# Performance work log

Measured on AMD Instinct MI355X. Metric: run time of the kernel, lower is better.

Reference implementation:

```python
import jax, jax.numpy as jnp
import numpy as np

B, C, H, W = 4, 256, 64, 64
CP = C // 4  # embedding_channels, k=4 hardcoded
# branch index -> (key-stream i, query/value-stream j); streams: 0=t,1=b,2=m
IIDX = np.array([0, 0, 0, 1, 1, 1, 2, 2, 2])  # which stream feeds k
JIDX = np.array([0, 1, 2, 0, 1, 2, 0, 1, 2])  # which stream feeds q and v


def setup_inputs() -> dict:
    key = jax.random.key(0)
    ks = jax.random.split(key, 6)
    scale = 0.05
    return {
        "t": jax.random.normal(ks[0], (B, C, H, W), jnp.float32),
        "b": jax.random.normal(ks[1], (B, C, H, W), jnp.float32),
        "m": jax.random.normal(ks[2], (B, C, H, W), jnp.float32),
        "W_qkv": jax.random.normal(ks[3], (9, C, C), jnp.float32) * scale,
        "W_red": jax.random.normal(ks[4], (9, CP, C), jnp.float32) * scale,
        "W_rec": jax.random.normal(ks[5], (9, C, CP), jnp.float32) * scale,
    }


def _pool(x):
    # ChannelAttention: global avg pool + global max pool -> [B, C']
    return jnp.mean(x, axis=(2, 3)) + jnp.max(x, axis=(2, 3))


def _channel_attention(q, k, v, w_red, w_rec):
    # q,k,v: [B,C,H,W]; w_red: [C',C]; w_rec: [C,C']
    ori = q + k + v
    red = lambda x: jax.nn.relu(jnp.einsum("bchw,ec->behw", x, w_red))
    qr, kr, vr = red(q), red(k), red(v)
    f = _pool(kr)  # key   -> [B,C']
    g = _pool(qr)  # query -> [B,C']
    h = _pool(vr)  # value -> [B,C']
    # s = f^T g : [B,C',C']; softmax over dim=1 (rows), per torch nn.Softmax(dim=1)
    s = f[:, :, None] * g[:, None, :]
    beta = jax.nn.softmax(s, axis=1)
    vout = jnp.einsum("bi,bij->bj", h, beta)  # [B,C']
    # recovery 1x1 conv on [B,C',1,1]; bilinear upsample from 1x1 == broadcast
    o = jax.nn.sigmoid(jnp.einsum("be,ce->bc", vout, w_rec))  # [B,C]
    return o[:, :, None, None] * ori


def reference(t, b, m, W_qkv, W_red, W_rec):
    x = jnp.stack([t, b, m])  # [3,B,C,H,W]
    Wp = W_qkv.reshape(3, 3, C, C)  # [stream, (q,k,v), C_out, C_in]
    proj = jnp.einsum("sbchw,sjec->sjbehw", x, Wp)  # [3,3,B,C,H,W]
    Q, K, V = proj[:, 0], proj[:, 1], proj[:, 2]  # each [3,B,C,H,W]
    q9, k9, v9 = Q[JIDX], K[IIDX], V[JIDX]  # [9,B,C,H,W]
    outs = jax.vmap(_channel_attention)(q9, k9, v9, W_red, W_rec)
    return outs.sum(axis=0)
```

## Files before the change

### kernel.cpp

```cpp
#include <hip/hip_runtime.h>

#define Bn 4
#define Cn 256
#define HWn 4096
#define CPn 64
#define MP 640

typedef unsigned short u16;
typedef unsigned int u32;

using short8  = __attribute__((ext_vector_type(8))) short;
using floatx4 = __attribute__((ext_vector_type(4))) float;

static __device__ __forceinline__ u16 f2bf(float f) {
    union { float f; u32 u; } v; v.f = f;
    u32 r = (v.u + 0x7FFFu + ((v.u >> 16) & 1u)) >> 16;
    return (u16)r;
}

static __device__ __forceinline__ void gld16(const u16* g, u16* l) {
    __builtin_amdgcn_global_load_lds(
        (const __attribute__((address_space(1))) u32*)g,
        (__attribute__((address_space(3))) u32*)l, 16, 0, 0);
}


__global__ __launch_bounds__(256) void convert_transpose(
    const float* __restrict__ Tt, const float* __restrict__ Bt, const float* __restrict__ Mt,
    u16* __restrict__ xT)
{
    const int s  = blockIdx.z, b = blockIdx.y;
    const int ct = blockIdx.x & 3, hwt = blockIdx.x >> 2;
    const int c0 = ct * 64, hw0 = hwt * 64;
    const float* X = (s == 0 ? Tt : (s == 1 ? Bt : Mt)) + (size_t)b * Cn * HWn;

    __shared__ u16 T[64][72];
    const int t = threadIdx.x;
    const int cl = t >> 2, q = t & 3;

    const float* src = X + (size_t)(c0 + cl) * HWn + hw0 + q * 16;
    #pragma unroll
    for (int u = 0; u < 4; ++u) {
        const float4 v = *(const float4*)(src + u * 4);
        T[cl][q * 16 + u * 4 + 0] = f2bf(v.x);
        T[cl][q * 16 + u * 4 + 1] = f2bf(v.y);
        T[cl][q * 16 + u * 4 + 2] = f2bf(v.z);
        T[cl][q * 16 + u * 4 + 3] = f2bf(v.w);
    }
    __syncthreads();

    const int wl = t >> 2;
    u16* dst = xT + ((size_t)((s * Bn + b) * HWn) + hw0 + wl) * Cn + c0 + q * 16;
    #pragma unroll
    for (int u = 0; u < 2; ++u) {
        u32 w0 = (u32)T[q * 16 + u * 8 + 0][wl] | ((u32)T[q * 16 + u * 8 + 1][wl] << 16);
        u32 w1 = (u32)T[q * 16 + u * 8 + 2][wl] | ((u32)T[q * 16 + u * 8 + 3][wl] << 16);
        u32 w2 = (u32)T[q * 16 + u * 8 + 4][wl] | ((u32)T[q * 16 + u * 8 + 5][wl] << 16);
        u32 w3 = (u32)T[q * 16 + u * 8 + 6][wl] | ((u32)T[q * 16 + u * 8 + 7][wl] << 16);
        uint4 pk = {w0, w1, w2, w3};
        *(uint4*)(dst + u * 8) = pk;
    }
}

__global__ __launch_bounds__(256) void compose_red(
    const float* __restrict__ Wqkv, const float* __restrict__ Wred,
    u16* __restrict__ CWp)
{
    const int s  = blockIdx.z;
    const int tt = blockIdx.y / 3, m3 = blockIdx.y % 3;
    const int c0 = blockIdx.x * 64;
    const int idx = (tt == 1) ? (3 * s + m3) : (3 * m3 + s);

    const float* A = Wred + (size_t)idx * CPn * Cn;
    const float* Bm = Wqkv + (size_t)(3 * s + tt) * Cn * Cn;

    __shared__ float As[16][64];
    __shared__ float Bs[16][64];
    const int t = threadIdx.x;
    const int ty = t >> 4, tx = t & 15;
    float acc[4][4] = {};

    for (int k0 = 0; k0 < Cn; k0 += 16) {
        {
            const int r = t >> 2, eq = (t & 3) * 4;
            const float4 a = *(const float4*)(A + (size_t)r * Cn + k0 + eq);
            As[eq + 0][r] = a.x; As[eq + 1][r] = a.y; As[eq + 2][r] = a.z; As[eq + 3][r] = a.w;
        }
        {
            const int r = t >> 4, cq = (t & 15) * 4;
            *(float4*)(&Bs[r][cq]) = *(const float4*)(Bm + (size_t)(k0 + r) * Cn + c0 + cq);
        }
        __syncthreads();
        #pragma unroll
        for (int k = 0; k < 16; ++k) {
            const float4 a4 = *(const float4*)(&As[k][ty * 4]);
            const float4 b4 = *(const float4*)(&Bs[k][tx * 4]);
            const float a[4] = {a4.x, a4.y, a4.z, a4.w};
            const float bb[4] = {b4.x, b4.y, b4.z, b4.w};
            #pragma unroll
            for (int i = 0; i < 4; ++i)
                #pragma unroll
                for (int j = 0; j < 4; ++j)
                    acc[i][j] = fmaf(a[i], bb[j], acc[i][j]);
        }
        __syncthreads();
    }

    u16* out = CWp + (size_t)s * MP * Cn;
    #pragma unroll
    for (int i = 0; i < 4; ++i) {
        const int row = tt * 192 + m3 * 64 + ty * 4 + i;
        unsigned long long pk =
            (unsigned long long)f2bf(acc[i][0]) |
            ((unsigned long long)f2bf(acc[i][1]) << 16) |
            ((unsigned long long)f2bf(acc[i][2]) << 32) |
            ((unsigned long long)f2bf(acc[i][3]) << 48);
        *(unsigned long long*)(out + (size_t)row * Cn + c0 + tx * 4) = pk;
    }
}

__global__ __launch_bounds__(256, 2) void redpool_mfma(
    const u16* __restrict__ xT, const u16* __restrict__ CWp,
    float* __restrict__ Psum, float* __restrict__ Pmax)
{
    const int s  = blockIdx.z;
    const int mt = blockIdx.x >> 7, nt = blockIdx.x & 127;
    const int m0 = mt * 128, n0 = nt * 128;

    const u16* Ap = CWp + (size_t)s * MP * Cn;
    const u16* Bp = xT + (size_t)s * Bn * HWn * Cn;

    __shared__ __align__(16) u16 As[32 * 512];
    __shared__ __align__(16) u16 Bs[32 * 512];

    const int t = threadIdx.x;
    const int w = t >> 6, lane = t & 63;
    const int l15 = lane & 15, q = lane >> 4;
    const int rb = (w >> 1) * 64, cb = (w & 1) * 64;

    floatx4 acc[4][4] = {};

    #pragma unroll
    for (int it = 0; it < 2; ++it) {
        const int k0 = it * 128;
        const u16* Asrc = Ap + (size_t)(m0 + l15) * Cn + k0 + q * 8;
        const u16* Bsrc = Bp + (size_t)(n0 + l15) * Cn + k0 + q * 8;
        #pragma unroll
        for (int pi = 0; pi < 8; ++pi) {
            const int p = w * 8 + pi;
            const size_t roff = (size_t)((p >> 2) * 16);
            gld16(Asrc + roff * Cn + (p & 3) * 32, &As[p * 512]);
            gld16(Bsrc + roff * Cn + (p & 3) * 32, &Bs[p * 512]);
        }
        __syncthreads();
        #pragma unroll
        for (int kk = 0; kk < 4; ++kk) {
            short8 af[4], bf[4];
            #pragma unroll
            for (int i = 0; i < 4; ++i)
                af[i] = *(const short8*)&As[((((w >> 1) * 4 + i) << 2) + kk) * 512 + lane * 8];
            #pragma unroll
            for (int j = 0; j < 4; ++j)
                bf[j] = *(const short8*)&Bs[((((w & 1) * 4 + j) << 2) + kk) * 512 + lane * 8];
            #pragma unroll
            for (int i = 0; i < 4; ++i)
                #pragma unroll
                for (int j = 0; j < 4; ++j)
                    acc[i][j] = __builtin_amdgcn_mfma_f32_16x16x32_bf16(af[i], bf[j], acc[i][j], 0, 0, 0);
        }
        __syncthreads();
    }

    float* Lsum = (float*)As;
    float* Lmax = Lsum + 256;
    const int wi = w & 1;
    #pragma unroll
    for (int i = 0; i < 4; ++i) {
        #pragma unroll
        for (int r = 0; r < 4; ++r) {
            float rs = 0.f, rm = 0.f;
            #pragma unroll
            for (int j = 0; j < 4; ++j) {
                const float v = fmaxf(acc[i][j][r], 0.f);
                rs += v; rm = fmaxf(rm, v);
            }
            #pragma unroll
            for (int off = 1; off < 16; off <<= 1) {
                rs += __shfl_xor(rs, off);
                rm = fmaxf(rm, __shfl_xor(rm, off));
            }
            if (l15 == 0) {
                const int lr = rb + 16 * i + q * 4 + r;
                Lsum[wi * 128 + lr] = rs;
                Lmax[wi * 128 + lr] = rm;
            }
        }
    }
    __syncthreads();
    if (t < 128) {
        const int R = m0 + t;
        const int b = nt >> 5, chunk = nt & 31;
        const size_t o = (((size_t)s * MP + R) * Bn + b) * 32 + chunk;
        Psum[o] = Lsum[t] + Lsum[128 + t];
        Pmax[o] = fmaxf(Lmax[t], Lmax[128 + t]);
    }
}

__global__ __launch_bounds__(256) void attn_small(
    const float* __restrict__ Psum, const float* __restrict__ Pmax,
    const float* __restrict__ Wrec,
    float* __restrict__ coefA, float* __restrict__ coefK)
{
    const int idx = blockIdx.x / Bn;
    const int bb  = blockIdx.x % Bn;
    __shared__ float ff[CPn], gg[CPn], hh[CPn], vout[CPn];
    const int t = threadIdx.x;

    if (t < CPn) {
        float v[3];
        #pragma unroll
        for (int tt = 0; tt < 3; ++tt) {
            const int s_ = (tt == 1) ? idx / 3 : idx % 3;
            const int m3 = (tt == 1) ? idx % 3 : idx / 3;
            const int R  = tt * 192 + m3 * 64 + t;
            const size_t base = (((size_t)s_ * MP + R) * Bn + bb) * 32;
            float sm = 0.f, mx = 0.f;
            #pragma unroll
            for (int u = 0; u < 32; ++u) {
                sm += Psum[base + u];
                mx = fmaxf(mx, Pmax[base + u]);
            }
            v[tt] = sm * (1.0f / HWn) + mx;
        }
        gg[t] = v[0];
        ff[t] = v[1];
        hh[t] = v[2];
    }
    __syncthreads();

    if (t < CPn) {
        const float gj = gg[t];
        float mx = -1e30f;
        for (int i = 0; i < CPn; ++i) mx = fmaxf(mx, ff[i] * gj);
        float den = 0.f, num = 0.f;
        for (int i = 0; i < CPn; ++i) {
            const float e = expf(ff[i] * gj - mx);
            den += e;
            num += hh[i] * e;
        }
        vout[t] = num / den;
    }
    __syncthreads();

    {
        const float* wr = Wrec + ((size_t)idx * Cn + t) * CPn;
        float a = 0.f;
        for (int e = 0; e < CPn; ++e) a += vout[e] * wr[e];
        const float o = 1.0f / (1.0f + expf(-a));
        const int sj = idx % 3;
        const int si = idx / 3;
        atomicAdd(coefA + (sj * Bn + bb) * Cn + t, o);
        atomicAdd(coefK + (si * Bn + bb) * Cn + t, o);
    }
}

__global__ __launch_bounds__(256) void build_M(
    const float* __restrict__ Wqkv,
    const float* __restrict__ coefA, const float* __restrict__ coefK,
    u16* __restrict__ Mm)
{
    const int s = blockIdx.x >> 8, m = blockIdx.x & 255;
    const int b = blockIdx.y;
    const int t = threadIdx.x;
    const float cA = coefA[(s * Bn + b) * Cn + m];
    const float cK = coefK[(s * Bn + b) * Cn + m];
    const float wq = Wqkv[((size_t)(3 * s + 0) * Cn + m) * Cn + t];
    const float wk = Wqkv[((size_t)(3 * s + 1) * Cn + m) * Cn + t];
    const float wv = Wqkv[((size_t)(3 * s + 2) * Cn + m) * Cn + t];
    Mm[((size_t)(b * 256 + m)) * 768 + s * 256 + t] = f2bf(cA * (wq + wv) + cK * wk);
}

__global__ __launch_bounds__(256, 2) void final_mfma(
    const u16* __restrict__ xT, const u16* __restrict__ Mm,
    float* __restrict__ out)
{
    const int b  = blockIdx.y;
    const int mt = blockIdx.x >> 5, nt = blockIdx.x & 31;
    const int m0 = mt * 128, n0 = nt * 128;

    __shared__ __align__(16) u16 As[32 * 512];
    __shared__ __align__(16) u16 Bs[32 * 512];

    const int t = threadIdx.x;
    const int w = t >> 6, lane = t & 63;
    const int l15 = lane & 15, q = lane >> 4;
    const int rb = (w >> 1) * 64, cb = (w & 1) * 64;

    const u16* Apb = Mm + (size_t)(b * 256 + m0) * 768;

    floatx4 acc[4][4] = {};

    for (int k0 = 0; k0 < 768; k0 += 128) {
        const int s = k0 >> 8, c0 = k0 & 255;
        const u16* Asrc = Apb + (size_t)l15 * 768 + k0 + q * 8;
        const u16* Bsrc = xT + ((size_t)((s * Bn + b) * HWn) + n0 + l15) * Cn + c0 + q * 8;
        #pragma unroll
        for (int pi = 0; pi < 8; ++pi) {
            const int p = w * 8 + pi;
            const size_t roff = (size_t)((p >> 2) * 16);
            gld16(Asrc + roff * 768 + (p & 3) * 32, &As[p * 512]);
            gld16(Bsrc + roff * Cn + (p & 3) * 32, &Bs[p * 512]);
        }
        __syncthreads();
        #pragma unroll
        for (int kk = 0; kk < 4; ++kk) {
            short8 af[4], bf[4];
            #pragma unroll
            for (int i = 0; i < 4; ++i)
                af[i] = *(const short8*)&As[((((w >> 1) * 4 + i) << 2) + kk) * 512 + lane * 8];
            #pragma unroll
            for (int j = 0; j < 4; ++j)
                bf[j] = *(const short8*)&Bs[((((w & 1) * 4 + j) << 2) + kk) * 512 + lane * 8];
            #pragma unroll
            for (int i = 0; i < 4; ++i)
                #pragma unroll
                for (int j = 0; j < 4; ++j)
                    acc[i][j] = __builtin_amdgcn_mfma_f32_16x16x32_bf16(af[i], bf[j], acc[i][j], 0, 0, 0);
        }
        __syncthreads();
    }

    #pragma unroll
    for (int i = 0; i < 4; ++i)
        #pragma unroll
        for (int j = 0; j < 4; ++j)
            #pragma unroll
            for (int r = 0; r < 4; ++r) {
                const int row = m0 + rb + i * 16 + q * 4 + r;
                const int col = n0 + cb + j * 16 + l15;
                out[((size_t)(b * 256) + row) * HWn + col] = acc[i][j][r];
            }
}

extern "C" void kernel_launch(void* const* d_in, const int* in_sizes, int n_in,
                              void* d_out, int out_size, void* d_ws, size_t ws_size,
                              hipStream_t stream)
{
    const float* Tt   = (const float*)d_in[0];
    const float* Bt   = (const float*)d_in[1];
    const float* Mt   = (const float*)d_in[2];
    const float* Wqkv = (const float*)d_in[3];
    const float* Wred = (const float*)d_in[4];
    const float* Wrec = (const float*)d_in[5];
    float* out = (float*)d_out;

    unsigned char* p = (unsigned char*)d_ws;
    u16* xT = (u16*)p;            p += (size_t)3 * Bn * HWn * Cn * 2;
    u16* Mm = (u16*)p;            p += (size_t)Bn * 256 * 768 * 2;
    float* Psum = (float*)p;      p += (size_t)3 * MP * Bn * 32 * 4;
    float* Pmax = (float*)p;      p += (size_t)3 * MP * Bn * 32 * 4;
    unsigned char* zbase = p;
    u16* CWp = (u16*)p;           p += (size_t)3 * MP * Cn * 2;
    float* coefA = (float*)p;     p += (size_t)3 * Bn * Cn * 4;
    float* coefK = (float*)p;     p += (size_t)3 * Bn * Cn * 4;
    const size_t zbytes = (size_t)(p - zbase);

    hipMemsetAsync(zbase, 0, zbytes, stream);

    compose_red      <<<dim3(4, 9, 3),    256, 0, stream>>>(Wqkv, Wred, CWp);
    convert_transpose<<<dim3(256, Bn, 3), 256, 0, stream>>>(Tt, Bt, Mt, xT);
    redpool_mfma     <<<dim3(640, 1, 3),  256, 0, stream>>>(xT, CWp, Psum, Pmax);
    attn_small       <<<9 * Bn,           256, 0, stream>>>(Psum, Pmax, Wrec, coefA, coefK);
    build_M          <<<dim3(768, Bn),    256, 0, stream>>>(Wqkv, coefA, coefK, Mm);
    final_mfma       <<<dim3(64, Bn),     256, 0, stream>>>(xT, Mm, out);
}
```

Before: 198.0 us.

## Merge prep kernels, persistent A-in-registers redpool, double-buffer final GEMM, drop memset

```diff
diff --git a/kernel.cpp b/kernel.cpp
--- a/kernel.cpp
+++ b/kernel.cpp
@@ -25,58 +25,59 @@
 }
 
 
-__global__ __launch_bounds__(256) void convert_transpose(
+__global__ __launch_bounds__(256) void prep(
     const float* __restrict__ Tt, const float* __restrict__ Bt, const float* __restrict__ Mt,
-    u16* __restrict__ xT)
-{
-    const int s  = blockIdx.z, b = blockIdx.y;
-    const int ct = blockIdx.x & 3, hwt = blockIdx.x >> 2;
-    const int c0 = ct * 64, hw0 = hwt * 64;
-    const float* X = (s == 0 ? Tt : (s == 1 ? Bt : Mt)) + (size_t)b * Cn * HWn;
-
+    const float* __restrict__ Wqkv, const float* __restrict__ Wred,
+    u16* __restrict__ xT, u16* __restrict__ CWp)
+{
     __shared__ u16 T[64][72];
-    const int t = threadIdx.x;
-    const int cl = t >> 2, q = t & 3;
-
-    const float* src = X + (size_t)(c0 + cl) * HWn + hw0 + q * 16;
-    #pragma unroll
-    for (int u = 0; u < 4; ++u) {
-        const float4 v = *(const float4*)(src + u * 4);
-        T[cl][q * 16 + u * 4 + 0] = f2bf(v.x);
-        T[cl][q * 16 + u * 4 + 1] = f2bf(v.y);
-        T[cl][q * 16 + u * 4 + 2] = f2bf(v.z);
-        T[cl][q * 16 + u * 4 + 3] = f2bf(v.w);
-    }
-    __syncthreads();
-
-    const int wl = t >> 2;
-    u16* dst = xT + ((size_t)((s * Bn + b) * HWn) + hw0 + wl) * Cn + c0 + q * 16;
-    #pragma unroll
-    for (int u = 0; u < 2; ++u) {
-        u32 w0 = (u32)T[q * 16 + u * 8 + 0][wl] | ((u32)T[q * 16 + u * 8 + 1][wl] << 16);
-        u32 w1 = (u32)T[q * 16 + u * 8 + 2][wl] | ((u32)T[q * 16 + u * 8 + 3][wl] << 16);
-        u32 w2 = (u32)T[q * 16 + u * 8 + 4][wl] | ((u32)T[q * 16 + u * 8 + 5][wl] << 16);
-        u32 w3 = (u32)T[q * 16 + u * 8 + 6][wl] | ((u32)T[q * 16 + u * 8 + 7][wl] << 16);
-        uint4 pk = {w0, w1, w2, w3};
-        *(uint4*)(dst + u * 8) = pk;
-    }
-}
-
-__global__ __launch_bounds__(256) void compose_red(
-    const float* __restrict__ Wqkv, const float* __restrict__ Wred,
-    u16* __restrict__ CWp)
-{
-    const int s  = blockIdx.z;
-    const int tt = blockIdx.y / 3, m3 = blockIdx.y % 3;
-    const int c0 = blockIdx.x * 64;
-    const int idx = (tt == 1) ? (3 * s + m3) : (3 * m3 + s);
-
-    const float* A = Wred + (size_t)idx * CPn * Cn;
-    const float* Bm = Wqkv + (size_t)(3 * s + tt) * Cn * Cn;
-
     __shared__ float As[16][64];
     __shared__ float Bs[16][64];
     const int t = threadIdx.x;
+
+    if (blockIdx.z < 3) {
+        const int s  = blockIdx.z, b = blockIdx.y;
+        const int ct = blockIdx.x & 3, hwt = blockIdx.x >> 2;
+        const int c0 = ct * 64, hw0 = hwt * 64;
+        const float* X = (s == 0 ? Tt : (s == 1 ? Bt : Mt)) + (size_t)b * Cn * HWn;
+
+        const int cl = t >> 2, q = t & 3;
+        const float* src = X + (size_t)(c0 + cl) * HWn + hw0 + q * 16;
+        #pragma unroll
+        for (int u = 0; u < 4; ++u) {
+            const float4 v = *(const float4*)(src + u * 4);
+            T[cl][q * 16 + u * 4 + 0] = f2bf(v.x);
+            T[cl][q * 16 + u * 4 + 1] = f2bf(v.y);
+            T[cl][q * 16 + u * 4 + 2] = f2bf(v.z);
+            T[cl][q * 16 + u * 4 + 3] = f2bf(v.w);
+        }
+        __syncthreads();
+
+        const int wl = t >> 2;
+        u16* dst = xT + ((size_t)((s * Bn + b) * HWn) + hw0 + wl) * Cn + c0 + q * 16;
+        #pragma unroll
+        for (int u = 0; u < 2; ++u) {
+            u32 w0 = (u32)T[q * 16 + u * 8 + 0][wl] | ((u32)T[q * 16 + u * 8 + 1][wl] << 16);
+            u32 w1 = (u32)T[q * 16 + u * 8 + 2][wl] | ((u32)T[q * 16 + u * 8 + 3][wl] << 16);
+            u32 w2 = (u32)T[q * 16 + u * 8 + 4][wl] | ((u32)T[q * 16 + u * 8 + 5][wl] << 16);
+            u32 w3 = (u32)T[q * 16 + u * 8 + 6][wl] | ((u32)T[q * 16 + u * 8 + 7][wl] << 16);
+            uint4 pk = {w0, w1, w2, w3};
+            *(uint4*)(dst + u * 8) = pk;
+        }
+        return;
+    }
+
+    const int lin = blockIdx.y * 256 + blockIdx.x;
+    if (lin >= 108) return;
+    const int c0  = (lin & 3) * 64;
+    const int rest = lin >> 2;
+    const int y9 = rest % 9, s = rest / 9;
+    const int tt = y9 / 3, m3 = y9 % 3;
+    const int idx = (tt == 1) ? (3 * s + m3) : (3 * m3 + s);
+
+    const float* A  = Wred + (size_t)idx * CPn * Cn;
+    const float* Bm = Wqkv + (size_t)(3 * s + tt) * Cn * Cn;
+
     const int ty = t >> 4, tx = t & 15;
     float acc[4][4] = {};
 
@@ -106,7 +107,7 @@
         __syncthreads();
     }
 
-    u16* out = CWp + (size_t)s * MP * Cn;
+    u16* outp = CWp + (size_t)s * MP * Cn;
     #pragma unroll
     for (int i = 0; i < 4; ++i) {
         const int row = tt * 192 + m3 * 64 + ty * 4 + i;
@@ -115,219 +116,250 @@
             ((unsigned long long)f2bf(acc[i][1]) << 16) |
             ((unsigned long long)f2bf(acc[i][2]) << 32) |
             ((unsigned long long)f2bf(acc[i][3]) << 48);
-        *(unsigned long long*)(out + (size_t)row * Cn + c0 + tx * 4) = pk;
-    }
-}
-
-__global__ __launch_bounds__(256, 2) void redpool_mfma(
+        *(unsigned long long*)(outp + (size_t)row * Cn + c0 + tx * 4) = pk;
+    }
+}
+
+#define NSUB 16
+
+__global__ __launch_bounds__(256, 1) void redpool_mfma(
     const u16* __restrict__ xT, const u16* __restrict__ CWp,
     float* __restrict__ Psum, float* __restrict__ Pmax)
 {
-    const int s  = blockIdx.z;
-    const int mt = blockIdx.x >> 7, nt = blockIdx.x & 127;
-    const int m0 = mt * 128, n0 = nt * 128;
+    const int s   = blockIdx.z;
+    const int mt  = blockIdx.x >> 4, nch = blockIdx.x & 15;
+    const int m0  = mt * 128;
+    const int nbase = nch * 1024;
 
     const u16* Ap = CWp + (size_t)s * MP * Cn;
     const u16* Bp = xT + (size_t)s * Bn * HWn * Cn;
 
-    __shared__ __align__(16) u16 As[32 * 512];
-    __shared__ __align__(16) u16 Bs[32 * 512];
+    __shared__ __align__(16) u16 Bs[2][32 * 512];
+
+    const int t = threadIdx.x;
+    const int w = t >> 6, lane = t & 63;
+    const int l15 = lane & 15, q = lane >> 4;
+    const int wr = w >> 1, wc = w & 1;
+
+    short8 af[4][8];
+    {
+        const u16* Arow = Ap + (size_t)(m0 + wr * 64 + l15) * Cn + q * 8;
+        #pragma unroll
+        for (int i = 0; i < 4; ++i)
+            #pragma unroll
+            for (int kk = 0; kk < 8; ++kk)
+                af[i][kk] = *(const short8*)(Arow + (size_t)(i * 16) * Cn + kk * 32);
+    }
+
+    auto stageB = [&](int it, int buf) {
+        const u16* Bsrc = Bp + (size_t)(nbase + it * 64 + l15) * Cn + q * 8;
+        #pragma unroll
+        for (int pi = 0; pi < 8; ++pi) {
+            const int p = w * 8 + pi;
+            gld16(Bsrc + (size_t)((p >> 3) * 16) * Cn + (p & 7) * 32, &Bs[buf][p * 512]);
+        }
+    };
+    stageB(0, 0);
+
+    float rs[4][4] = {};
+    float rm[4][4] = {};
+
+    for (int it = 0; it < NSUB; ++it) {
+        __syncthreads();
+        if (it + 1 < NSUB) stageB(it + 1, (it + 1) & 1);
+        const u16* bb = Bs[it & 1];
+
+        floatx4 acc[4][2] = {};
+        #pragma unroll
+        for (int kk = 0; kk < 8; ++kk) {
+            short8 bf[2];
+            #pragma unroll
+            for (int j = 0; j < 2; ++j)
+                bf[j] = *(const short8*)&bb[((wc * 2 + j) * 8 + kk) * 512 + lane * 8];
+            #pragma unroll
+            for (int i = 0; i < 4; ++i)
+                #pragma unroll
+                for (int j = 0; j < 2; ++j)
+                    acc[i][j] = __builtin_amdgcn_mfma_f32_16x16x32_bf16(af[i][kk], bf[j], acc[i][j], 0, 0, 0);
+        }
+        #pragma unroll
+        for (int i = 0; i < 4; ++i)
+            #pragma unroll
+            for (int r = 0; r < 4; ++r) {
+                const float v0 = fmaxf(acc[i][0][r], 0.f);
+                const float v1 = fmaxf(acc[i][1][r], 0.f);
+                rs[i][r] += v0 + v1;
+                rm[i][r] = fmaxf(rm[i][r], fmaxf(v0, v1));
+            }
+    }
+
+    #pragma unroll
+    for (int i = 0; i < 4; ++i)
+        #pragma unroll
+        for (int r = 0; r < 4; ++r) {
+            #pragma unroll
+            for (int off = 1; off < 16; off <<= 1) {
+                rs[i][r] += __shfl_xor(rs[i][r], off);
+                rm[i][r] = fmaxf(rm[i][r], __shfl_xor(rm[i][r], off));
+            }
+        }
+
+    __syncthreads();
+    float* Lsum = (float*)&Bs[0][0];
+    float* Lmax = Lsum + 256;
+    if (l15 == 0) {
+        #pragma unroll
+        for (int i = 0; i < 4; ++i)
+            #pragma unroll
+            for (int r = 0; r < 4; ++r) {
+                const int row = wr * 64 + i * 16 + q * 4 + r;
+                Lsum[wc * 128 + row] = rs[i][r];
+                Lmax[wc * 128 + row] = rm[i][r];
+            }
+    }
+    __syncthreads();
+    if (t < 128) {
+        const int R = m0 + t;
+        const size_t o = ((size_t)s * MP + R) * 16 + nch;
+        Psum[o] = Lsum[t] + Lsum[128 + t];
+        Pmax[o] = fmaxf(Lmax[t], Lmax[128 + t]);
+    }
+}
+
+__global__ __launch_bounds__(64) void attn_small(
+    const float* __restrict__ Psum, const float* __restrict__ Pmax,
+    float* __restrict__ vout)
+{
+    const int idx = blockIdx.x / Bn;
+    const int bb  = blockIdx.x % Bn;
+    __shared__ float ff[CPn], gg[CPn], hh[CPn];
+    const int t = threadIdx.x;
+
+    float v[3];
+    #pragma unroll
+    for (int tt = 0; tt < 3; ++tt) {
+        const int s_ = (tt == 1) ? idx / 3 : idx % 3;
+        const int m3 = (tt == 1) ? idx % 3 : idx / 3;
+        const int R  = tt * 192 + m3 * 64 + t;
+        const size_t base = ((size_t)s_ * MP + R) * 16 + bb * 4;
+        float sm = 0.f, mx = 0.f;
+        #pragma unroll
+        for (int u = 0; u < 4; ++u) {
+            sm += Psum[base + u];
+            mx = fmaxf(mx, Pmax[base + u]);
+        }
+        v[tt] = sm * (1.0f / HWn) + mx;
+    }
+    gg[t] = v[0];
+    ff[t] = v[1];
+    hh[t] = v[2];
+    __syncthreads();
+
+    const float gj = gg[t];
+    float mx = -1e30f;
+    for (int i = 0; i < CPn; ++i) mx = fmaxf(mx, ff[i] * gj);
+    float den = 0.f, num = 0.f;
+    for (int i = 0; i < CPn; ++i) {
+        const float e = expf(ff[i] * gj - mx);
+        den += e;
+        num += hh[i] * e;
+    }
+    vout[((size_t)idx * Bn + bb) * CPn + t] = num / den;
+}
+
+__global__ __launch_bounds__(256) void build_M(
+    const float* __restrict__ Wqkv, const float* __restrict__ Wrec,
+    const float* __restrict__ vout, u16* __restrict__ Mm)
+{
+    const int s = blockIdx.x >> 8, m = blockIdx.x & 255;
+    const int b = blockIdx.y;
+    const int t = threadIdx.x;
+    __shared__ float cc[2];
+
+    if (t < CPn) {
+        float d[6];
+        #pragma unroll
+        for (int j = 0; j < 6; ++j) {
+            const int idx = (j < 3) ? (s + 3 * j) : (3 * s + (j - 3));
+            d[j] = vout[((size_t)idx * Bn + b) * CPn + t] *
+                   Wrec[((size_t)idx * Cn + m) * CPn + t];
+        }
+        #pragma unroll
+        for (int off = 32; off >= 1; off >>= 1)
+            #pragma unroll
+            for (int j = 0; j < 6; ++j)
+                d[j] += __shfl_xor(d[j], off);
+        if (t == 0) {
+            float cA = 0.f, cK = 0.f;
+            #pragma unroll
+            for (int j = 0; j < 3; ++j) {
+                cA += 1.0f / (1.0f + expf(-d[j]));
+                cK += 1.0f / (1.0f + expf(-d[j + 3]));
+            }
+            cc[0] = cA; cc[1] = cK;
+        }
+    }
+    __syncthreads();
+    const float cA = cc[0], cK = cc[1];
+    const float wq = Wqkv[((size_t)(3 * s + 0) * Cn + m) * Cn + t];
+    const float wk = Wqkv[((size_t)(3 * s + 1) * Cn + m) * Cn + t];
+    const float wv = Wqkv[((size_t)(3 * s + 2) * Cn + m) * Cn + t];
+    Mm[((size_t)(b * 256 + m)) * 768 + s * 256 + t] = f2bf(cA * (wq + wv) + cK * wk);
+}
+
+__global__ __launch_bounds__(256, 1) void final_mfma(
+    const u16* __restrict__ xT, const u16* __restrict__ Mm,
+    float* __restrict__ out)
+{
+    const int b  = blockIdx.y;
+    const int mt = blockIdx.x >> 5, nt = blockIdx.x & 31;
+    const int m0 = mt * 128, n0 = nt * 128;
+
+    __shared__ __align__(16) u16 As[2][32 * 512];
+    __shared__ __align__(16) u16 Bs[2][32 * 512];
 
     const int t = threadIdx.x;
     const int w = t >> 6, lane = t & 63;
     const int l15 = lane & 15, q = lane >> 4;
     const int rb = (w >> 1) * 64, cb = (w & 1) * 64;
 
-    floatx4 acc[4][4] = {};
-
-    #pragma unroll
-    for (int it = 0; it < 2; ++it) {
+    auto stage = [&](int it, int buf) {
         const int k0 = it * 128;
-        const u16* Asrc = Ap + (size_t)(m0 + l15) * Cn + k0 + q * 8;
-        const u16* Bsrc = Bp + (size_t)(n0 + l15) * Cn + k0 + q * 8;
+        const int s = k0 >> 8, c0 = k0 & 255;
+        const u16* Asrc = Mm + (size_t)(b * 256 + m0 + l15) * 768 + k0 + q * 8;
+        const u16* Bsrc = xT + ((size_t)((s * Bn + b) * HWn) + n0 + l15) * Cn + c0 + q * 8;
         #pragma unroll
         for (int pi = 0; pi < 8; ++pi) {
             const int p = w * 8 + pi;
             const size_t roff = (size_t)((p >> 2) * 16);
-            gld16(Asrc + roff * Cn + (p & 3) * 32, &As[p * 512]);
-            gld16(Bsrc + roff * Cn + (p & 3) * 32, &Bs[p * 512]);
-        }
+            gld16(Asrc + roff * 768 + (p & 3) * 32, &As[buf][p * 512]);
+            gld16(Bsrc + roff * Cn + (p & 3) * 32, &Bs[buf][p * 512]);
+        }
+    };
+    stage(0, 0);
+
+    floatx4 acc[4][4] = {};
+
+    for (int it = 0; it < 6; ++it) {
         __syncthreads();
+        if (it + 1 < 6) stage(it + 1, (it + 1) & 1);
+        const u16* as = As[it & 1];
+        const u16* bs = Bs[it & 1];
         #pragma unroll
         for (int kk = 0; kk < 4; ++kk) {
             short8 af[4], bf[4];
             #pragma unroll
             for (int i = 0; i < 4; ++i)
-                af[i] = *(const short8*)&As[((((w >> 1) * 4 + i) << 2) + kk) * 512 + lane * 8];
+                af[i] = *(const short8*)&as[((((w >> 1) * 4 + i) << 2) + kk) * 512 + lane * 8];
             #pragma unroll
             for (int j = 0; j < 4; ++j)
-                bf[j] = *(const short8*)&Bs[((((w & 1) * 4 + j) << 2) + kk) * 512 + lane * 8];
+                bf[j] = *(const short8*)&bs[((((w & 1) * 4 + j) << 2) + kk) * 512 + lane * 8];
             #pragma unroll
             for (int i = 0; i < 4; ++i)
                 #pragma unroll
                 for (int j = 0; j < 4; ++j)
                     acc[i][j] = __builtin_amdgcn_mfma_f32_16x16x32_bf16(af[i], bf[j], acc[i][j], 0, 0, 0);
         }
-        __syncthreads();
-    }
-
-    float* Lsum = (float*)As;
-    float* Lmax = Lsum + 256;
-    const int wi = w & 1;
-    #pragma unroll
-    for (int i = 0; i < 4; ++i) {
-        #pragma unroll
-        for (int r = 0; r < 4; ++r) {
-            float rs = 0.f, rm = 0.f;
-            #pragma unroll
-            for (int j = 0; j < 4; ++j) {
-                const float v = fmaxf(acc[i][j][r], 0.f);
-                rs += v; rm = fmaxf(rm, v);
-            }
-            #pragma unroll
-            for (int off = 1; off < 16; off <<= 1) {
-                rs += __shfl_xor(rs, off);
-                rm = fmaxf(rm, __shfl_xor(rm, off));
-            }
-            if (l15 == 0) {
-                const int lr = rb + 16 * i + q * 4 + r;
-                Lsum[wi * 128 + lr] = rs;
-                Lmax[wi * 128 + lr] = rm;
-            }
-        }
-    }
-    __syncthreads();
-    if (t < 128) {
-        const int R = m0 + t;
-        const int b = nt >> 5, chunk = nt & 31;
-        const size_t o = (((size_t)s * MP + R) * Bn + b) * 32 + chunk;
-        Psum[o] = Lsum[t] + Lsum[128 + t];
-        Pmax[o] = fmaxf(Lmax[t], Lmax[128 + t]);
-    }
-}
-
-__global__ __launch_bounds__(256) void attn_small(
-    const float* __restrict__ Psum, const float* __restrict__ Pmax,
-    const float* __restrict__ Wrec,
-    float* __restrict__ coefA, float* __restrict__ coefK)
-{
-    const int idx = blockIdx.x / Bn;
-    const int bb  = blockIdx.x % Bn;
-    __shared__ float ff[CPn], gg[CPn], hh[CPn], vout[CPn];
-    const int t = threadIdx.x;
-
-    if (t < CPn) {
-        float v[3];
-        #pragma unroll
-        for (int tt = 0; tt < 3; ++tt) {
-            const int s_ = (tt == 1) ? idx / 3 : idx % 3;
-            const int m3 = (tt == 1) ? idx % 3 : idx / 3;
-            const int R  = tt * 192 + m3 * 64 + t;
-            const size_t base = (((size_t)s_ * MP + R) * Bn + bb) * 32;
-            float sm = 0.f, mx = 0.f;
-            #pragma unroll
-            for (int u = 0; u < 32; ++u) {
-                sm += Psum[base + u];
-                mx = fmaxf(mx, Pmax[base + u]);
-            }
-            v[tt] = sm * (1.0f / HWn) + mx;
-        }
-        gg[t] = v[0];
-        ff[t] = v[1];
-        hh[t] = v[2];
-    }
-    __syncthreads();
-
-    if (t < CPn) {
-        const float gj = gg[t];
-        float mx = -1e30f;
-        for (int i = 0; i < CPn; ++i) mx = fmaxf(mx, ff[i] * gj);
-        float den = 0.f, num = 0.f;
-        for (int i = 0; i < CPn; ++i) {
-            const float e = expf(ff[i] * gj - mx);
-            den += e;
-            num += hh[i] * e;
-        }
-        vout[t] = num / den;
-    }
-    __syncthreads();
-
-    {
-        const float* wr = Wrec + ((size_t)idx * Cn + t) * CPn;
-        float a = 0.f;
-        for (int e = 0; e < CPn; ++e) a += vout[e] * wr[e];
-        const float o = 1.0f / (1.0f + expf(-a));
-        const int sj = idx % 3;
-        const int si = idx / 3;
-        atomicAdd(coefA + (sj * Bn + bb) * Cn + t, o);
-        atomicAdd(coefK + (si * Bn + bb) * Cn + t, o);
-    }
-}
-
-__global__ __launch_bounds__(256) void build_M(
-    const float* __restrict__ Wqkv,
-    const float* __restrict__ coefA, const float* __restrict__ coefK,
-    u16* __restrict__ Mm)
-{
-    const int s = blockIdx.x >> 8, m = blockIdx.x & 255;
-    const int b = blockIdx.y;
-    const int t = threadIdx.x;
-    const float cA = coefA[(s * Bn + b) * Cn + m];
-    const float cK = coefK[(s * Bn + b) * Cn + m];
-    const float wq = Wqkv[((size_t)(3 * s + 0) * Cn + m) * Cn + t];
-    const float wk = Wqkv[((size_t)(3 * s + 1) * Cn + m) * Cn + t];
-    const float wv = Wqkv[((size_t)(3 * s + 2) * Cn + m) * Cn + t];
-    Mm[((size_t)(b * 256 + m)) * 768 + s * 256 + t] = f2bf(cA * (wq + wv) + cK * wk);
-}
-
-__global__ __launch_bounds__(256, 2) void final_mfma(
-    const u16* __restrict__ xT, const u16* __restrict__ Mm,
-    float* __restrict__ out)
-{
-    const int b  = blockIdx.y;
-    const int mt = blockIdx.x >> 5, nt = blockIdx.x & 31;
-    const int m0 = mt * 128, n0 = nt * 128;
-
-    __shared__ __align__(16) u16 As[32 * 512];
-    __shared__ __align__(16) u16 Bs[32 * 512];
-
-    const int t = threadIdx.x;
-    const int w = t >> 6, lane = t & 63;
-    const int l15 = lane & 15, q = lane >> 4;
-    const int rb = (w >> 1) * 64, cb = (w & 1) * 64;
-
-    const u16* Apb = Mm + (size_t)(b * 256 + m0) * 768;
-
-    floatx4 acc[4][4] = {};
-
-    for (int k0 = 0; k0 < 768; k0 += 128) {
-        const int s = k0 >> 8, c0 = k0 & 255;
-        const u16* Asrc = Apb + (size_t)l15 * 768 + k0 + q * 8;
-        const u16* Bsrc = xT + ((size_t)((s * Bn + b) * HWn) + n0 + l15) * Cn + c0 + q * 8;
-        #pragma unroll
-        for (int pi = 0; pi < 8; ++pi) {
-            const int p = w * 8 + pi;
-            const size_t roff = (size_t)((p >> 2) * 16);
-            gld16(Asrc + roff * 768 + (p & 3) * 32, &As[p * 512]);
-            gld16(Bsrc + roff * Cn + (p & 3) * 32, &Bs[p * 512]);
-        }
-        __syncthreads();
-        #pragma unroll
-        for (int kk = 0; kk < 4; ++kk) {
-            short8 af[4], bf[4];
-            #pragma unroll
-            for (int i = 0; i < 4; ++i)
-                af[i] = *(const short8*)&As[((((w >> 1) * 4 + i) << 2) + kk) * 512 + lane * 8];
-            #pragma unroll
-            for (int j = 0; j < 4; ++j)
-                bf[j] = *(const short8*)&Bs[((((w & 1) * 4 + j) << 2) + kk) * 512 + lane * 8];
-            #pragma unroll
-            for (int i = 0; i < 4; ++i)
-                #pragma unroll
-                for (int j = 0; j < 4; ++j)
-                    acc[i][j] = __builtin_amdgcn_mfma_f32_16x16x32_bf16(af[i], bf[j], acc[i][j], 0, 0, 0);
-        }
-        __syncthreads();
     }
 
     #pragma unroll
@@ -357,20 +389,14 @@
     unsigned char* p = (unsigned char*)d_ws;
     u16* xT = (u16*)p;            p += (size_t)3 * Bn * HWn * Cn * 2;
     u16* Mm = (u16*)p;            p += (size_t)Bn * 256 * 768 * 2;
-    float* Psum = (float*)p;      p += (size_t)3 * MP * Bn * 32 * 4;
-    float* Pmax = (float*)p;      p += (size_t)3 * MP * Bn * 32 * 4;
-    unsigned char* zbase = p;
     u16* CWp = (u16*)p;           p += (size_t)3 * MP * Cn * 2;
-    float* coefA = (float*)p;     p += (size_t)3 * Bn * Cn * 4;
-    float* coefK = (float*)p;     p += (size_t)3 * Bn * Cn * 4;
-    const size_t zbytes = (size_t)(p - zbase);
-
-    hipMemsetAsync(zbase, 0, zbytes, stream);
-
-    compose_red      <<<dim3(4, 9, 3),    256, 0, stream>>>(Wqkv, Wred, CWp);
-    convert_transpose<<<dim3(256, Bn, 3), 256, 0, stream>>>(Tt, Bt, Mt, xT);
-    redpool_mfma     <<<dim3(640, 1, 3),  256, 0, stream>>>(xT, CWp, Psum, Pmax);
-    attn_small       <<<9 * Bn,           256, 0, stream>>>(Psum, Pmax, Wrec, coefA, coefK);
-    build_M          <<<dim3(768, Bn),    256, 0, stream>>>(Wqkv, coefA, coefK, Mm);
-    final_mfma       <<<dim3(64, Bn),     256, 0, stream>>>(xT, Mm, out);
-}
+    float* Psum = (float*)p;      p += (size_t)3 * MP * 16 * 4;
+    float* Pmax = (float*)p;      p += (size_t)3 * MP * 16 * 4;
+    float* vout = (float*)p;      p += (size_t)9 * Bn * CPn * 4;
+
+    prep        <<<dim3(256, Bn, 4), 256, 0, stream>>>(Tt, Bt, Mt, Wqkv, Wred, xT, CWp);
+    redpool_mfma<<<dim3(80, 1, 3),   256, 0, stream>>>(xT, CWp, Psum, Pmax);
+    attn_small  <<<9 * Bn,            64, 0, stream>>>(Psum, Pmax, vout);
+    build_M     <<<dim3(768, Bn),    256, 0, stream>>>(Wqkv, Wrec, vout, Mm);
+    final_mfma  <<<dim3(64, Bn),     256, 0, stream>>>(xT, Mm, out);
+}
```

Result: faster. 170.3 us (-14.0%).
